# Kernel tuning notes

Measured on AMD Instinct MI355X. Metric: run time of the kernel, lower is better.

Reference implementation:

```python
import jax, jax.numpy as jnp
import numpy as np

QK_NOPE = 128  # qk_nope_head_dim; softmax scale uses nope+rope head dim
EPS = 1e-6

def _rmsnorm(x, w):
    return x * jax.lax.rsqrt(jnp.mean(x * x, axis=-1, keepdims=True) + EPS) * w

def _deinterleave(x):
    # torch: view(..., d//2, 2).transpose(-1, -2).reshape(..., d)
    return jnp.concatenate([x[..., 0::2], x[..., 1::2]], axis=-1)

def _rotate_half(x):
    h = x.shape[-1] // 2
    return jnp.concatenate([-x[..., h:], x[..., :h]], axis=-1)

def _rope_cos_sin(position_ids, dim, theta=10000.0):
    inv_freq = 1.0 / (theta ** (jnp.arange(0, dim, 2, dtype=jnp.float32) / dim))  # [dim/2]
    freqs = position_ids.astype(jnp.float32)[..., None] * inv_freq               # [B,S,dim/2]
    emb = jnp.concatenate([freqs, freqs], axis=-1)                               # [B,S,dim]
    return jnp.cos(emb)[:, None], jnp.sin(emb)[:, None]                          # [B,1,S,dim]


def setup_inputs() -> dict:
    B, S, HID, H = 2, 1024, 4096, 32
    QL, KVL, ROPE, V = 1536, 512, 64, 128
    key = jax.random.key(0)
    ks = jax.random.split(key, 8)
    def w(k, shape, fan_in):
        return jax.random.normal(k, shape, jnp.float32) * (fan_in ** -0.5)
    hidden_states = jax.random.normal(ks[0], (B, S, HID), jnp.float32)
    causal = jnp.tril(jnp.ones((S, S), bool))
    attention_mask = jnp.where(causal, 0.0, -1e9).astype(jnp.float32)[None, None]  # [1,1,S,S]
    position_ids = jnp.broadcast_to(jnp.arange(S, dtype=jnp.int32), (B, S))
    return {
        'hidden_states': hidden_states,
        'attention_mask': attention_mask,
        'position_ids': position_ids,
        'w_q_a': w(ks[1], (HID, QL), HID),
        'q_a_ln_w': jnp.ones((QL,), jnp.float32),
        'q_rope': w(ks[2], (QL, H * ROPE), QL),
        'fusedqk': w(ks[3], (H, QL, KVL), QL),
        'w_kv_a': w(ks[4], (HID, KVL + ROPE), HID),
        'kv_a_ln_w': jnp.ones((KVL,), jnp.float32),
        'per_head_v_up': w(ks[5], (H, KVL, V), KVL),
        'w_o': w(ks[6], (H * V, HID), H * V),
    }


def _mla_forward(hidden_states, attention_mask, position_ids, w_q_a, q_a_ln_w,
                 q_rope, fusedqk, w_kv_a, kv_a_ln_w, per_head_v_up, w_o):
    B, S, _ = hidden_states.shape
    H, QL, KVL = fusedqk.shape
    ROPE = q_rope.shape[1] // H
    # compressed KV projection (MQA): split into latent kv and rope key part
    ckv = hidden_states @ w_kv_a                              # [B,S,KVL+ROPE]
    kva = _rmsnorm(ckv[..., :KVL], kv_a_ln_w)                 # [B,S,KVL]
    k_pe = ckv[..., KVL:][:, None]                            # [B,1,S,ROPE]
    # low-rank query
    q_a = _rmsnorm(hidden_states @ w_q_a, q_a_ln_w)           # [B,S,QL]
    q_pe = (q_a @ q_rope).reshape(B, S, H, ROPE).transpose(0, 2, 1, 3)  # [B,H,S,ROPE]
    # interleaved RoPE (deinterleave then standard rotate-half)
    cos, sin = _rope_cos_sin(position_ids, ROPE)
    qd = _deinterleave(q_pe)
    kd = _deinterleave(k_pe)
    q_pe = qd * cos + _rotate_half(qd) * sin                  # [B,H,S,ROPE]
    k_pe = kd * cos + _rotate_half(kd) * sin                  # [B,1,S,ROPE]
    # absorbed query: q_a @ (q_up @ k_up^T), precomputed as fusedqk
    q_abs = jnp.einsum('bsr,hrc->bhsc', q_a, fusedqk)         # [B,H,S,KVL]
    query = jnp.concatenate([q_abs, q_pe], axis=-1)           # [B,H,S,KVL+ROPE]
    keys = jnp.concatenate([kva, k_pe[:, 0]], axis=-1)        # [B,S,KVL+ROPE]
    scale = (QK_NOPE + ROPE) ** -0.5
    scores = jnp.einsum('bhsd,btd->bhst', query, keys) * scale + attention_mask
    attn = jax.nn.softmax(scores, axis=-1)                    # [B,H,S,S]
    ctx = jnp.einsum('bhst,btc->bhsc', attn, kva)             # [B,H,S,KVL]
    out = jnp.einsum('bhsc,hcv->bhsv', ctx, per_head_v_up)    # [B,H,S,V]
    out = out.transpose(0, 2, 1, 3).reshape(B, S, -1)         # [B,S,H*V]
    return out @ w_o                                          # [B,S,HID]


def reference(hidden_states, attention_mask, position_ids, w_q_a, q_a_ln_w,
              q_rope, fusedqk, w_kv_a, kv_a_ln_w, per_head_v_up, w_o):
    return _mla_forward(hidden_states, attention_mask, position_ids, w_q_a,
                        q_a_ln_w, q_rope, fusedqk, w_kv_a, kv_a_ln_w,
                        per_head_v_up, w_o)
```

## Files before the change

### kernel.cpp

```cpp
#include <hip/hip_runtime.h>


typedef __attribute__((ext_vector_type(8))) short s16x8;
typedef __attribute__((ext_vector_type(4))) float f32x4;

__device__ __forceinline__ float bf2f(unsigned short u) {
  union { unsigned int i; float f; } v; v.i = ((unsigned int)u) << 16; return v.f;
}
__device__ __forceinline__ unsigned short f2bf(float f) {
  union { float f; unsigned int i; } v; v.f = f;
  unsigned int x = v.i;
  x += 0x7fffu + ((x >> 16) & 1u);
  return (unsigned short)(x >> 16);
}

__device__ __forceinline__ void async16(const unsigned short* g, unsigned short* l) {
  __builtin_amdgcn_global_load_lds(
      (const __attribute__((address_space(1))) unsigned int*)g,
      (__attribute__((address_space(3))) unsigned int*)l, 16, 0, 0);
}

__global__ __launch_bounds__(256) void conv_bf16(
    const float* __restrict__ s, unsigned short* __restrict__ d)
{
  const long long i = ((long long)blockIdx.x * 256 + threadIdx.x) * 8;
  float4 a = *(const float4*)(s + i);
  float4 b = *(const float4*)(s + i + 4);
  union { uint4 v; unsigned short u[8]; } o;
  o.u[0] = f2bf(a.x); o.u[1] = f2bf(a.y); o.u[2] = f2bf(a.z); o.u[3] = f2bf(a.w);
  o.u[4] = f2bf(b.x); o.u[5] = f2bf(b.y); o.u[6] = f2bf(b.z); o.u[7] = f2bf(b.w);
  *(uint4*)(d + i) = o.v;
}

__global__ __launch_bounds__(256) void transpose_w(
    const float* __restrict__ src, unsigned short* __restrict__ dst,
    int R, int C, long long sS, long long sD)
{
  __shared__ unsigned short tile[32][36];
  src += (long long)blockIdx.z * sS;
  dst += (long long)blockIdx.z * sD;
  const int c0 = blockIdx.x * 32, r0 = blockIdx.y * 32;
  const int tid = threadIdx.x;
  const int rr = tid >> 3, cc4 = (tid & 7) * 4;
  if (c0 < C) {
    float4 v = *(const float4*)(src + (long long)(r0 + rr) * C + c0 + cc4);
    tile[cc4 + 0][rr] = f2bf(v.x); tile[cc4 + 1][rr] = f2bf(v.y);
    tile[cc4 + 2][rr] = f2bf(v.z); tile[cc4 + 3][rr] = f2bf(v.w);
  } else {
#pragma unroll
    for (int j = 0; j < 4; ++j) tile[cc4 + j][rr] = 0;
  }
  __syncthreads();
  const int cr = tid >> 3, rc4 = (tid & 7) * 4;
  union { uint2 v; unsigned short u[4]; } o;
#pragma unroll
  for (int j = 0; j < 4; ++j) o.u[j] = tile[cr][rc4 + j];
  *(uint2*)(dst + (long long)(c0 + cr) * R + r0 + rc4) = o.v;
}

template<int ODT>
__global__ __launch_bounds__(256) void gemm128(
    const unsigned short* __restrict__ A, const unsigned short* __restrict__ Bt,
    void* __restrict__ Cv, int K, int lda, int ldb, int ldc, int batH,
    long long sAb, long long sAh, long long sBb, long long sBh,
    long long sCb, long long sCh)
{
  const int z = blockIdx.z;
  const int bz = z / batH, hz = z % batH;
  A  += (long long)bz * sAb + (long long)hz * sAh;
  Bt += (long long)bz * sBb + (long long)hz * sBh;
  const long long co = (long long)bz * sCb + (long long)hz * sCh;

  __shared__ __align__(16) unsigned short As[128 * 32];
  __shared__ __align__(16) unsigned short Bs[128 * 32];

  const int tid = threadIdx.x, w = tid >> 6, lane = tid & 63;
  const int quad = lane >> 4, ml = lane & 15;
  const int wm = (w >> 1) * 64, wn = (w & 1) * 64;
  const int m0 = blockIdx.y * 128, n0 = blockIdx.x * 128;

  const int r0 = tid >> 2, k8 = (tid & 3) * 8;
  const unsigned short* Ag0 = A  + (long long)(m0 + r0)      * lda + k8;
  const unsigned short* Ag1 = A  + (long long)(m0 + r0 + 64) * lda + k8;
  const unsigned short* Bg0 = Bt + (long long)(n0 + r0)      * ldb + k8;
  const unsigned short* Bg1 = Bt + (long long)(n0 + r0 + 64) * ldb + k8;
  unsigned short* la0 = &As[tid * 8];
  unsigned short* la1 = &As[(tid + 256) * 8];
  unsigned short* lb0 = &Bs[tid * 8];
  unsigned short* lb1 = &Bs[(tid + 256) * 8];

  f32x4 acc[4][4] = {};

  for (int k0 = 0; k0 < K; k0 += 32) {
    __syncthreads();
    async16(Ag0 + k0, la0);
    async16(Ag1 + k0, la1);
    async16(Bg0 + k0, lb0);
    async16(Bg1 + k0, lb1);
    __syncthreads();

    s16x8 af[4], bf[4];
#pragma unroll
    for (int mi = 0; mi < 4; ++mi)
      af[mi] = *(const s16x8*)(&As[(wm + mi * 16 + ml) * 32 + quad * 8]);
#pragma unroll
    for (int ni = 0; ni < 4; ++ni)
      bf[ni] = *(const s16x8*)(&Bs[(wn + ni * 16 + ml) * 32 + quad * 8]);
#pragma unroll
    for (int mi = 0; mi < 4; ++mi)
#pragma unroll
      for (int ni = 0; ni < 4; ++ni)
        acc[mi][ni] = __builtin_amdgcn_mfma_f32_16x16x32_bf16(af[mi], bf[ni], acc[mi][ni], 0, 0, 0);
  }

#pragma unroll
  for (int mi = 0; mi < 4; ++mi)
#pragma unroll
    for (int ni = 0; ni < 4; ++ni)
#pragma unroll
      for (int r = 0; r < 4; ++r) {
        const int row = m0 + wm + mi * 16 + quad * 4 + r;
        const int col = n0 + wn + ni * 16 + ml;
        if (ODT)
          ((unsigned short*)Cv)[co + (long long)row * ldc + col] = f2bf(acc[mi][ni][r]);
        else
          ((float*)Cv)[co + (long long)row * ldc + col] = acc[mi][ni][r];
      }
}

__global__ __launch_bounds__(256) void kv_norm_rope(
    const float* __restrict__ ckv, const float* __restrict__ w,
    const int* __restrict__ pos_ids, unsigned short* __restrict__ keys)
{
  __shared__ float sbuf[4];
  const int r = blockIdx.x, tid = threadIdx.x;
  const float* row = ckv + (long long)r * 640;
  float x0 = row[tid], x1 = row[256 + tid];
  float ss = x0 * x0 + x1 * x1;
#pragma unroll
  for (int o = 32; o; o >>= 1) ss += __shfl_xor(ss, o);
  if ((tid & 63) == 0) sbuf[tid >> 6] = ss;
  __syncthreads();
  const float tot = sbuf[0] + sbuf[1] + sbuf[2] + sbuf[3];
  const float rms = rsqrtf(tot / 512.0f + 1e-6f);
  unsigned short* kr = keys + (long long)r * 576;
  kr[tid]       = f2bf(x0 * rms * w[tid]);
  kr[256 + tid] = f2bf(x1 * rms * w[256 + tid]);
  if (tid < 32) {
    const float pos = (float)pos_ids[r];
    const float invf = exp2f(-0.41524101186098287f * (float)tid);
    float sn, c; sincosf(pos * invf, &sn, &c);
    const float a0 = row[512 + 2 * tid], a1 = row[512 + 2 * tid + 1];
    kr[512 + tid] = f2bf(a0 * c - a1 * sn);
    kr[544 + tid] = f2bf(a1 * c + a0 * sn);
  }
}

__global__ __launch_bounds__(256) void q_norm(
    const float* __restrict__ qa_f32, const float* __restrict__ w,
    unsigned short* __restrict__ qa_bf)
{
  __shared__ float sbuf[4];
  const int r = blockIdx.x, tid = threadIdx.x;
  const float* row = qa_f32 + (long long)r * 1536;
  float x[6]; float ss = 0.f;
#pragma unroll
  for (int j = 0; j < 6; ++j) { x[j] = row[tid + 256 * j]; ss += x[j] * x[j]; }
#pragma unroll
  for (int o = 32; o; o >>= 1) ss += __shfl_xor(ss, o);
  if ((tid & 63) == 0) sbuf[tid >> 6] = ss;
  __syncthreads();
  const float tot = sbuf[0] + sbuf[1] + sbuf[2] + sbuf[3];
  const float rms = rsqrtf(tot / 1536.0f + 1e-6f);
#pragma unroll
  for (int j = 0; j < 6; ++j) {
    const int idx = tid + 256 * j;
    qa_bf[(long long)r * 1536 + idx] = f2bf(x[j] * rms * w[idx]);
  }
}

__global__ __launch_bounds__(256) void rope_q(
    const unsigned short* __restrict__ qpe, const int* __restrict__ pos_ids,
    unsigned short* __restrict__ query)
{
  const int r = blockIdx.x;
  const int b = r >> 10, s = r & 1023;
  const float pos = (float)pos_ids[r];
  for (int p = threadIdx.x; p < 1024; p += 256) {
    const int h = p >> 5, i = p & 31;
    const float invf = exp2f(-0.41524101186098287f * (float)i);
    float sn, c; sincosf(pos * invf, &sn, &c);
    const float a0 = bf2f(qpe[(long long)r * 2048 + h * 64 + 2 * i]);
    const float a1 = bf2f(qpe[(long long)r * 2048 + h * 64 + 2 * i + 1]);
    const long long qrow = ((long long)(b * 32 + h) * 1024 + s) * 576;
    query[qrow + 512 + i] = f2bf(a0 * c - a1 * sn);
    query[qrow + 544 + i] = f2bf(a1 * c + a0 * sn);
  }
}

__global__ __launch_bounds__(256) void transpose_keys(
    const unsigned short* __restrict__ keys, unsigned short* __restrict__ keysT)
{
  __shared__ unsigned short tile[32][36];
  const int tid = threadIdx.x;
  const int t0 = blockIdx.x * 32, d0 = blockIdx.y * 32, b = blockIdx.z;
  const int r = tid >> 3, c4 = (tid & 7) * 4;
  *(uint2*)(&tile[r][c4]) =
      *(const uint2*)(keys + ((long long)(b * 1024 + t0 + r) * 576 + d0 + c4));
  __syncthreads();
  unsigned short v[4];
#pragma unroll
  for (int j = 0; j < 4; ++j) v[j] = tile[c4 + j][r];
  *(uint2*)(keysT + ((long long)(b * 512 + d0 + r) * 1024 + t0 + c4)) = *(uint2*)v;
}

__global__ __launch_bounds__(512, 2) void flash_mfma(
    const unsigned short* __restrict__ query,
    const unsigned short* __restrict__ keys,
    const unsigned short* __restrict__ keysT,
    unsigned short* __restrict__ ctx)
{
  __shared__ __align__(16) unsigned short Ks[2][32 * 640];
  __shared__ __align__(16) unsigned short Ps[2][8][640];
  __shared__ float alpha_s[2][128];
  __shared__ float l_s[128];
  __shared__ __align__(16) int rflag[2][8];

  const int tid = threadIdx.x, w = tid >> 6, lane = tid & 63;
  const int quad = lane >> 4, ml = lane & 15;
  const int bid = blockIdx.x;
  const int bh = bid & 63;
  const int qt = 7 - (bid >> 6);
  const int q0 = qt * 128;
  const int b = bh >> 5;
  const float scale = 0.07216878364870323f;

  const unsigned short* kb  = keys  + (long long)b * 1024 * 576;
  const unsigned short* vtb = keysT + (long long)b * 512 * 1024;

  const unsigned short* qg =
      query + ((long long)bh * 1024 + q0 + w * 16 + ml) * 576 + quad * 8;
  s16x8 qf[18];
#pragma unroll
  for (int ks = 0; ks < 18; ++ks) qf[ks] = *(const s16x8*)(qg + ks * 32);

  int koff[5];
#pragma unroll
  for (int j = 0; j < 5; ++j) {
    const int idx = tid + 512 * j;
    const int row = idx / 80;
    const int c16 = idx - row * 80;
    koff[j] = row * 576 + ((c16 ^ (row & 7)) << 3);
  }
  char* ldsb = (char*)&Ks[0][0] + tid * 16;
  auto stage = [&](int t, int buf) {
    const long long toff = (long long)t * 18432;
    char* lb = ldsb + buf * 40960;
#pragma unroll
    for (int j = 0; j < 5; ++j)
      async16(kb + toff + koff[j], (unsigned short*)(lb + j * 8192));
  };

  const int e3 = ml & 7;
  const int qi = q0 + w * 16 + ml;
  const int ntile = 4 * qt + 4;

  float m = -1e30f, l = 0.f;
  f32x4 o[8][4] = {};

  stage(0, 0);

  for (int ti = 0; ti < ntile; ++ti) {
    const int buf = ti & 1;
    const int t0 = ti * 32;

    if (ti + 1 < ntile) {
      stage(ti + 1, buf ^ 1);
      asm volatile("s_waitcnt vmcnt(5)" ::: "memory");
    } else {
      asm volatile("s_waitcnt vmcnt(0)" ::: "memory");
    }
    __builtin_amdgcn_sched_barrier(0);
    __builtin_amdgcn_s_barrier();
    __builtin_amdgcn_sched_barrier(0);

    const bool wdead = (t0 > q0 + w * 16 + 15);
    if (!wdead) {
      const unsigned short* Kb = &Ks[buf][0];
      f32x4 sc0 = {}, sc1 = {};
#pragma unroll
      for (int ks = 0; ks < 18; ++ks) {
        const int xr = ((ks * 4 + quad) ^ e3) << 3;
        s16x8 k0 = *(const s16x8*)(Kb + ml * 640 + xr);
        s16x8 k1 = *(const s16x8*)(Kb + (16 + ml) * 640 + xr);
        sc0 = __builtin_amdgcn_mfma_f32_16x16x32_bf16(k0, qf[ks], sc0, 0, 0, 0);
        sc1 = __builtin_amdgcn_mfma_f32_16x16x32_bf16(k1, qf[ks], sc1, 0, 0, 0);
      }

      float p[8]; float mx = -1e30f;
      const bool tail = (t0 + 31 > q0 + w * 16);
#pragma unroll
      for (int r = 0; r < 4; ++r) {
        float v0 = sc0[r] * scale, v1 = sc1[r] * scale;
        if (tail) {
          if (t0 + quad * 4 + r > qi)      v0 = -1e30f;
          if (t0 + 16 + quad * 4 + r > qi) v1 = -1e30f;
        }
        p[r] = v0; p[4 + r] = v1;
        mx = fmaxf(mx, fmaxf(v0, v1));
      }
      mx = fmaxf(mx, __shfl_xor(mx, 16));
      mx = fmaxf(mx, __shfl_xor(mx, 32));

      float alpha = 1.0f;
      int resc = 0;
      if (!__all(mx - m <= 8.0f)) {
        const float mn = fmaxf(m, mx);
        alpha = __expf(m - mn);
        m = mn;
        l *= alpha;
        resc = 1;
      }
      if (lane == 0) rflag[buf][w] = resc;
      if (quad == 0) alpha_s[buf][w * 16 + ml] = alpha;

      float ps = 0.f;
#pragma unroll
      for (int j = 0; j < 8; ++j) { p[j] = __expf(p[j] - m); ps += p[j]; }
      ps += __shfl_xor(ps, 16);
      ps += __shfl_xor(ps, 32);
      l += ps;

#pragma unroll
      for (int c = 0; c < 2; ++c) {
        union { unsigned short u[4]; uint2 v; } pk;
        pk.u[0] = f2bf(p[c * 4 + 0]); pk.u[1] = f2bf(p[c * 4 + 1]);
        pk.u[2] = f2bf(p[c * 4 + 2]); pk.u[3] = f2bf(p[c * 4 + 3]);
        *(uint2*)(&Ps[buf][w][ml * 40 + c * 16 + quad * 4]) = pk.v;
      }
    } else {
      if (lane == 0) rflag[buf][w] = 0;
      if (quad == 0) alpha_s[buf][w * 16 + ml] = 1.0f;
    }

    const unsigned short* vg =
        vtb + (long long)(w * 64 + ml) * 1024 + t0 + quad * 8;
    s16x8 vf[4];
#pragma unroll
    for (int nt = 0; nt < 4; ++nt) vf[nt] = *(const s16x8*)(vg + nt * 16 * 1024);

    asm volatile("s_waitcnt lgkmcnt(0)" ::: "memory");
    __builtin_amdgcn_sched_barrier(0);
    __builtin_amdgcn_s_barrier();
    __builtin_amdgcn_sched_barrier(0);

    const int4 ra = *(const int4*)&rflag[buf][0];
    const int4 rb = *(const int4*)&rflag[buf][4];
    if (ra.x | ra.y | ra.z | ra.w | rb.x | rb.y | rb.z | rb.w) {
#pragma unroll
      for (int qc = 0; qc < 8; ++qc)
#pragma unroll
        for (int r = 0; r < 4; ++r) {
          const float a = alpha_s[buf][qc * 16 + quad * 4 + r];
#pragma unroll
          for (int nt = 0; nt < 4; ++nt) o[qc][nt][r] *= a;
        }
    }

#pragma unroll
    for (int qc = 0; qc < 8; ++qc) {
      if (t0 > q0 + qc * 16 + 15) continue;
      s16x8 pa = *(const s16x8*)(&Ps[buf][qc][ml * 40 + quad * 8]);
#pragma unroll
      for (int nt = 0; nt < 4; ++nt)
        o[qc][nt] = __builtin_amdgcn_mfma_f32_16x16x32_bf16(pa, vf[nt], o[qc][nt], 0, 0, 0);
    }
  }

  if (quad == 0) l_s[w * 16 + ml] = l;
  __syncthreads();

  unsigned short* cb = ctx + ((long long)bh * 1024 + q0) * 512 + w * 64 + ml;
#pragma unroll
  for (int qc = 0; qc < 8; ++qc)
#pragma unroll
    for (int r = 0; r < 4; ++r) {
      const float linv = 1.0f / l_s[qc * 16 + quad * 4 + r];
      unsigned short* crow = cb + (long long)(qc * 16 + quad * 4 + r) * 512;
#pragma unroll
      for (int nt = 0; nt < 4; ++nt)
        crow[nt * 16] = f2bf(o[qc][nt][r] * linv);
    }
}

extern "C" void kernel_launch(void* const* d_in, const int* in_sizes, int n_in,
                              void* d_out, int out_size, void* d_ws, size_t ws_size,
                              hipStream_t stream)
{
  (void)in_sizes; (void)n_in; (void)out_size; (void)ws_size;
  const float* hs      = (const float*)d_in[0];
  const int*   pos     = (const int*)d_in[2];
  const float* w_q_a   = (const float*)d_in[3];
  const float* q_a_ln  = (const float*)d_in[4];
  const float* q_rope  = (const float*)d_in[5];
  const float* fusedqk = (const float*)d_in[6];
  const float* w_kv_a  = (const float*)d_in[7];
  const float* kv_ln   = (const float*)d_in[8];
  const float* v_up    = (const float*)d_in[9];
  const float* w_o     = (const float*)d_in[10];
  char* ws = (char*)d_ws;

  unsigned short* woT    = (unsigned short*)(ws + 0);
  unsigned short* vupT   = (unsigned short*)(ws + 33554432);
  unsigned short* keys   = (unsigned short*)(ws + 37748736);
  unsigned short* keysT  = (unsigned short*)(ws + 40108032);
  unsigned short* ctx    = (unsigned short*)(ws + 42205184);
  unsigned short* fqkT   = (unsigned short*)(ws + 42205184);
  unsigned short* qab    = (unsigned short*)(ws + 92536832);
  unsigned short* qpe    = (unsigned short*)(ws + 99828288);
  unsigned short* hsb    = (unsigned short*)(ws + 92536832);
  unsigned short* query  = (unsigned short*)(ws + 109314048);
  unsigned short* wqT    = (unsigned short*)(ws + 109314048);
  unsigned short* wkvT   = (unsigned short*)(ws + 121896960);
  unsigned short* qropeT = (unsigned short*)(ws + 127139840);
  float*          ckv    = (float*)(ws + 133431296);
  float*          qaf    = (float*)(ws + 138674176);
  unsigned short* outh   = (unsigned short*)(ws + 109314048);

  const dim3 blk(256);

  conv_bf16<<<dim3(4096), blk, 0, stream>>>(hs, hsb);
  transpose_w<<<dim3(20, 128, 1), blk, 0, stream>>>(w_kv_a, wkvT, 4096, 576, 0, 0);
  transpose_w<<<dim3(48, 128, 1), blk, 0, stream>>>(w_q_a, wqT, 4096, 1536, 0, 0);
  transpose_w<<<dim3(64, 48, 1), blk, 0, stream>>>(q_rope, qropeT, 1536, 2048, 0, 0);
  transpose_w<<<dim3(16, 48, 32), blk, 0, stream>>>(fusedqk, fqkT, 1536, 512,
      (long long)1536 * 512, (long long)512 * 1536);
  transpose_w<<<dim3(4, 16, 32), blk, 0, stream>>>(v_up, vupT, 512, 128,
      (long long)512 * 128, (long long)128 * 512);
  transpose_w<<<dim3(128, 128, 1), blk, 0, stream>>>(w_o, woT, 4096, 4096, 0, 0);

  gemm128<0><<<dim3(5, 16, 1), blk, 0, stream>>>(hsb, wkvT, (void*)ckv,
      4096, 4096, 4096, 640, 1, 0, 0, 0, 0, 0, 0);
  kv_norm_rope<<<dim3(2048), blk, 0, stream>>>(ckv, kv_ln, pos, keys);
  transpose_keys<<<dim3(32, 16, 2), blk, 0, stream>>>(keys, keysT);
  gemm128<0><<<dim3(12, 16, 1), blk, 0, stream>>>(hsb, wqT, (void*)qaf,
      4096, 4096, 4096, 1536, 1, 0, 0, 0, 0, 0, 0);
  q_norm<<<dim3(2048), blk, 0, stream>>>(qaf, q_a_ln, qab);
  gemm128<1><<<dim3(16, 16, 1), blk, 0, stream>>>(qab, qropeT, (void*)qpe,
      1536, 1536, 1536, 2048, 1, 0, 0, 0, 0, 0, 0);
  rope_q<<<dim3(2048), blk, 0, stream>>>(qpe, pos, query);
  gemm128<1><<<dim3(4, 8, 64), blk, 0, stream>>>(qab, fqkT, (void*)query,
      1536, 1536, 1536, 576, 32,
      (long long)1024 * 1536, 0, 0, (long long)512 * 1536,
      (long long)32 * 1024 * 576, (long long)1024 * 576);
  flash_mfma<<<dim3(512), dim3(512), 0, stream>>>(query, keys, keysT, ctx);
  gemm128<1><<<dim3(1, 8, 64), blk, 0, stream>>>(ctx, vupT, (void*)outh,
      512, 512, 512, 4096, 32,
      (long long)32 * 1024 * 512, (long long)1024 * 512, 0, (long long)128 * 512,
      (long long)1024 * 4096, 128);
  gemm128<0><<<dim3(32, 16, 1), blk, 0, stream>>>(outh, woT, d_out,
      4096, 4096, 4096, 4096, 1, 0, 0, 0, 0, 0, 0);
}
```

Baseline: 1.009 ms.

## Add 128x256 tile GEMM with split B staging for fusedqk and output projections

Adds a 512-thread GEMM kernel with a 128x256 output tile whose B-tile load is split into two halves. The second half is prefetched between the two MFMA phases, so loads overlap compute. The fused-qk query GEMM and the output projection now use it, to raise operand reuse per block and cut launch count. It also wraps the MFMA loops in the flash attention kernel with s_setprio raises. Risks are lower occupancy from the larger tiles and extra LDS use, plus fewer blocks for the 4096x4096 projection.

New measurement: 1.055 ms. 4.6% more time.

```diff
diff --git a/kernel.cpp b/kernel.cpp
--- a/kernel.cpp
+++ b/kernel.cpp
@@ -125,6 +125,134 @@
           ((unsigned short*)Cv)[co + (long long)row * ldc + col] = f2bf(acc[mi][ni][r]);
         else
           ((float*)Cv)[co + (long long)row * ldc + col] = acc[mi][ni][r];
+      }
+}
+
+template<int ODT>
+__global__ __launch_bounds__(512) void gemm256(
+    const unsigned short* __restrict__ A, const unsigned short* __restrict__ Bt,
+    void* __restrict__ Cv, int K, int lda, int ldb, int ldc, int batH,
+    long long sAb, long long sAh, long long sBb, long long sBh,
+    long long sCb, long long sCh)
+{
+  __shared__ __align__(16) unsigned short As[2 * 128 * 64];
+  __shared__ __align__(16) unsigned short Bs[2 * 256 * 64];
+
+  const int z = blockIdx.z;
+  const int bz = z / batH, hz = z % batH;
+  A  += (long long)bz * sAb + (long long)hz * sAh;
+  Bt += (long long)bz * sBb + (long long)hz * sBh;
+  const long long co = (long long)bz * sCb + (long long)hz * sCh;
+
+  const int tid = threadIdx.x, w = tid >> 6, lane = tid & 63;
+  const int quad = lane >> 4, ml = lane & 15;
+  const int wr = w >> 2, wc = w & 3;
+  const int e3 = ml & 7;
+  const int m0 = blockIdx.y * 128, n0 = blockIdx.x * 256;
+
+  const int srow_ = tid >> 3;
+  const int es = srow_ & 7;
+  const int scs = ((tid & 7) ^ es) << 3;
+  const long long gA0 = (long long)(m0 + srow_)       * lda + scs;
+  const long long gA1 = (long long)(m0 + 64 + srow_)  * lda + scs;
+  const long long gB0 = (long long)(n0 + srow_)       * ldb + scs;
+  const long long gB1 = (long long)(n0 + 64 + srow_)  * ldb + scs;
+  const long long gB2 = (long long)(n0 + 128 + srow_) * ldb + scs;
+  const long long gB3 = (long long)(n0 + 192 + srow_) * ldb + scs;
+
+  auto stageA = [&](int kt, int nb) {
+    async16(A + gA0 + kt * 64, &As[nb * 8192 + tid * 8]);
+    async16(A + gA1 + kt * 64, &As[nb * 8192 + 4096 + tid * 8]);
+  };
+  auto stageBlo = [&](int kt, int nb) {
+    async16(Bt + gB0 + kt * 64, &Bs[nb * 16384 + tid * 8]);
+    async16(Bt + gB1 + kt * 64, &Bs[nb * 16384 + 4096 + tid * 8]);
+  };
+  auto stageBhi = [&](int kt, int nb) {
+    async16(Bt + gB2 + kt * 64, &Bs[nb * 16384 + 8192 + tid * 8]);
+    async16(Bt + gB3 + kt * 64, &Bs[nb * 16384 + 12288 + tid * 8]);
+  };
+
+  f32x4 acc[4][4] = {};
+  const int NT = K >> 6;
+
+  stageA(0, 0); stageBlo(0, 0); stageBhi(0, 0);
+
+  for (int t = 0; t < NT; ++t) {
+    const int buf = t & 1, nb = buf ^ 1;
+
+    if (t + 1 < NT) {
+      stageA(t + 1, nb);
+      stageBlo(t + 1, nb);
+      asm volatile("s_waitcnt vmcnt(4)" ::: "memory");
+    } else {
+      asm volatile("s_waitcnt vmcnt(0)" ::: "memory");
+    }
+    __builtin_amdgcn_sched_barrier(0);
+    __builtin_amdgcn_s_barrier();
+    __builtin_amdgcn_sched_barrier(0);
+
+    const unsigned short* Ab = &As[buf * 8192];
+    const unsigned short* Bb = &Bs[buf * 16384];
+    s16x8 a[4][2], b0[2][2];
+#pragma unroll
+    for (int mf = 0; mf < 4; ++mf)
+#pragma unroll
+      for (int ks = 0; ks < 2; ++ks)
+        a[mf][ks] = *(const s16x8*)(Ab + (wr * 64 + mf * 16 + ml) * 64 +
+                                    (((ks * 4 + quad) ^ e3) << 3));
+#pragma unroll
+    for (int nf = 0; nf < 2; ++nf)
+#pragma unroll
+      for (int ks = 0; ks < 2; ++ks)
+        b0[nf][ks] = *(const s16x8*)(Bb + (wc * 64 + nf * 16 + ml) * 64 +
+                                     (((ks * 4 + quad) ^ e3) << 3));
+    __builtin_amdgcn_s_setprio(1);
+#pragma unroll
+    for (int mf = 0; mf < 4; ++mf)
+#pragma unroll
+      for (int nf = 0; nf < 2; ++nf) {
+        acc[mf][nf] = __builtin_amdgcn_mfma_f32_16x16x32_bf16(a[mf][0], b0[nf][0], acc[mf][nf], 0, 0, 0);
+        acc[mf][nf] = __builtin_amdgcn_mfma_f32_16x16x32_bf16(a[mf][1], b0[nf][1], acc[mf][nf], 0, 0, 0);
+      }
+    __builtin_amdgcn_s_setprio(0);
+    __builtin_amdgcn_s_barrier();
+
+    if (t + 1 < NT) stageBhi(t + 1, nb);
+    s16x8 b1[2][2];
+#pragma unroll
+    for (int nf = 0; nf < 2; ++nf)
+#pragma unroll
+      for (int ks = 0; ks < 2; ++ks)
+        b1[nf][ks] = *(const s16x8*)(Bb + (wc * 64 + (nf + 2) * 16 + ml) * 64 +
+                                     (((ks * 4 + quad) ^ e3) << 3));
+    __builtin_amdgcn_s_setprio(1);
+#pragma unroll
+    for (int mf = 0; mf < 4; ++mf)
+#pragma unroll
+      for (int nf = 0; nf < 2; ++nf) {
+        acc[mf][nf + 2] = __builtin_amdgcn_mfma_f32_16x16x32_bf16(a[mf][0], b1[nf][0], acc[mf][nf + 2], 0, 0, 0);
+        acc[mf][nf + 2] = __builtin_amdgcn_mfma_f32_16x16x32_bf16(a[mf][1], b1[nf][1], acc[mf][nf + 2], 0, 0, 0);
+      }
+    __builtin_amdgcn_s_setprio(0);
+    asm volatile("s_waitcnt lgkmcnt(0)" ::: "memory");
+    __builtin_amdgcn_sched_barrier(0);
+    __builtin_amdgcn_s_barrier();
+    __builtin_amdgcn_sched_barrier(0);
+  }
+
+#pragma unroll
+  for (int mf = 0; mf < 4; ++mf)
+#pragma unroll
+    for (int nf = 0; nf < 4; ++nf)
+#pragma unroll
+      for (int r = 0; r < 4; ++r) {
+        const int row = m0 + wr * 64 + mf * 16 + quad * 4 + r;
+        const int col = n0 + wc * 64 + nf * 16 + ml;
+        if (ODT)
+          ((unsigned short*)Cv)[co + (long long)row * ldc + col] = f2bf(acc[mf][nf][r]);
+        else
+          ((float*)Cv)[co + (long long)row * ldc + col] = acc[mf][nf][r];
       }
 }
 
@@ -288,6 +416,7 @@
     if (!wdead) {
       const unsigned short* Kb = &Ks[buf][0];
       f32x4 sc0 = {}, sc1 = {};
+      __builtin_amdgcn_s_setprio(1);
 #pragma unroll
       for (int ks = 0; ks < 18; ++ks) {
         const int xr = ((ks * 4 + quad) ^ e3) << 3;
@@ -296,6 +425,7 @@
         sc0 = __builtin_amdgcn_mfma_f32_16x16x32_bf16(k0, qf[ks], sc0, 0, 0, 0);
         sc1 = __builtin_amdgcn_mfma_f32_16x16x32_bf16(k1, qf[ks], sc1, 0, 0, 0);
       }
+      __builtin_amdgcn_s_setprio(0);
 
       float p[8]; float mx = -1e30f;
       const bool tail = (t0 + 31 > q0 + w * 16);
@@ -367,6 +497,7 @@
         }
     }
 
+    __builtin_amdgcn_s_setprio(1);
 #pragma unroll
     for (int qc = 0; qc < 8; ++qc) {
       if (t0 > q0 + qc * 16 + 15) continue;
@@ -375,6 +506,7 @@
       for (int nt = 0; nt < 4; ++nt)
         o[qc][nt] = __builtin_amdgcn_mfma_f32_16x16x32_bf16(pa, vf[nt], o[qc][nt], 0, 0, 0);
     }
+    __builtin_amdgcn_s_setprio(0);
   }
 
   if (quad == 0) l_s[w * 16 + ml] = l;
@@ -449,7 +581,7 @@
   gemm128<1><<<dim3(16, 16, 1), blk, 0, stream>>>(qab, qropeT, (void*)qpe,
       1536, 1536, 1536, 2048, 1, 0, 0, 0, 0, 0, 0);
   rope_q<<<dim3(2048), blk, 0, stream>>>(qpe, pos, query);
-  gemm128<1><<<dim3(4, 8, 64), blk, 0, stream>>>(qab, fqkT, (void*)query,
+  gemm256<1><<<dim3(2, 8, 64), dim3(512), 0, stream>>>(qab, fqkT, (void*)query,
       1536, 1536, 1536, 576, 32,
       (long long)1024 * 1536, 0, 0, (long long)512 * 1536,
       (long long)32 * 1024 * 576, (long long)1024 * 576);
@@ -458,6 +590,6 @@
       512, 512, 512, 4096, 32,
       (long long)32 * 1024 * 512, (long long)1024 * 512, 0, (long long)128 * 512,
       (long long)1024 * 4096, 128);
-  gemm128<0><<<dim3(32, 16, 1), blk, 0, stream>>>(outh, woT, d_out,
+  gemm256<0><<<dim3(16, 16, 1), dim3(512), 0, stream>>>(outh, woT, d_out,
       4096, 4096, 4096, 4096, 1, 0, 0, 0, 0, 0, 0);
 }
```
